# Kernel optimization log

Hardware: AMD Instinct MI355X
Metric: run time of the kernel (lower is better)

Reference implementation:

```python
import jax, jax.numpy as jnp
import numpy as np

N = 50000      # nodes (== nbr_nodes)
E = 800000     # edges
D_IN = 128
D_H = 128
D_OUT = 47
NOISE_RATE = 0.1
EPS = 1e-12


def _lin_init(key, out_f, in_f):
    # rough Glorot-style init for a PyG Linear weight [out_f, in_f]
    s = 1.0 / np.sqrt(in_f)
    return jax.random.uniform(key, (out_f, in_f), jnp.float32, -s, s)


def setup_inputs() -> dict:
    key = jax.random.key(0)
    ks = jax.random.split(key, 13)
    inp = {
        "x": jax.random.normal(ks[0], (N, D_IN), jnp.float32),
        "edge_index": jax.random.randint(ks[1], (2, E), 0, N, dtype=jnp.int32),
        "noise": jax.random.normal(ks[2], (N, D_IN), jnp.float32),
        # layer 0: in -> hidden
        "W_l0": _lin_init(ks[3], D_H, D_IN),
        "b_l0": jnp.zeros((D_H,), jnp.float32),
        "W_r0": _lin_init(ks[4], D_H, D_IN),
        # layer 1: hidden -> hidden
        "W_l1": _lin_init(ks[5], D_H, D_H),
        "b_l1": jnp.zeros((D_H,), jnp.float32),
        "W_r1": _lin_init(ks[6], D_H, D_H),
        # layer 2: hidden -> out
        "W_l2": _lin_init(ks[7], D_OUT, D_H),
        "b_l2": jnp.zeros((D_OUT,), jnp.float32),
        "W_r2": _lin_init(ks[8], D_OUT, D_H),
    }
    return inp


def _sage_conv(x, src, dst, W_l, b_l, W_r):
    # PyG SAGEConv with mean aggregation:
    #   out_i = W_l @ mean_{j in N(i)} x_j + b_l + W_r @ x_i
    msg = x[src]                                              # [E, d] gather
    ssum = jax.ops.segment_sum(msg, dst, num_segments=N)      # [N, d]
    cnt = jax.ops.segment_sum(jnp.ones((src.shape[0], 1), x.dtype), dst,
                              num_segments=N)                 # [N, 1]
    agg = ssum / jnp.maximum(cnt, 1.0)                        # mean; 0 for isolated nodes
    return agg @ W_l.T + b_l + x @ W_r.T


def _branch(x, src, dst, params):
    # stacked SAGEConv; relu after all but last layer; dropout is identity (eval mode)
    h = None
    n_layers = len(params)
    for i, (W_l, b_l, W_r) in enumerate(params):
        x = _sage_conv(x, src, dst, W_l, b_l, W_r)
        if i != n_layers - 1:
            x = jax.nn.relu(x)
            h = x
    return h, jax.nn.log_softmax(x, axis=1), x


def _add_noise(x, noise):
    # n_id=None path: x + sign(x) * F.normalize(noise, dim=1) * noise_rate
    norm = jnp.sqrt(jnp.sum(noise * noise, axis=1, keepdims=True))
    unit = noise / jnp.maximum(norm, EPS)
    return x + jnp.sign(x) * unit * NOISE_RATE


def reference(x, edge_index, noise,
              W_l0, b_l0, W_r0, W_l1, b_l1, W_r1, W_l2, b_l2, W_r2):
    src, dst = edge_index[0], edge_index[1]
    params = [(W_l0, b_l0, W_r0), (W_l1, b_l1, W_r1), (W_l2, b_l2, W_r2)]
    h_p, y_p, z_p = _branch(x, src, dst, params)
    h_n, y_n, z_n = _branch(_add_noise(x, noise), src, dst, params)
    return (h_p, y_p, z_p, h_n, y_n, z_n)
```

## Files before the change

### kernel.cpp

```cpp
#include <hip/hip_runtime.h>
#include <math.h>


typedef unsigned int uint;
typedef unsigned short ushort;
typedef unsigned char uchar;
typedef short bf16x8 __attribute__((ext_vector_type(8)));
typedef float f32x4 __attribute__((ext_vector_type(4)));

__device__ __forceinline__ ushort f2b(float f) {
  union { float f; uint u; } v; v.f = f;
  uint u = v.u;
  return (ushort)((u + 0x7FFFu + ((u >> 16) & 1u)) >> 16);
}
__device__ __forceinline__ float b2f_lo(uint u) {
  union { uint u; float f; } v; v.u = u << 16; return v.f;
}
__device__ __forceinline__ float b2f_hi(uint u) {
  union { uint u; float f; } v; v.u = u & 0xFFFF0000u; return v.f;
}

#if __has_builtin(__builtin_amdgcn_cvt_f32_fp8)
__device__ __forceinline__ float dec8_0(uint u) { return __builtin_amdgcn_cvt_f32_fp8(u, 0); }
__device__ __forceinline__ float dec8_1(uint u) { return __builtin_amdgcn_cvt_f32_fp8(u, 1); }
__device__ __forceinline__ float dec8_2(uint u) { return __builtin_amdgcn_cvt_f32_fp8(u, 2); }
__device__ __forceinline__ float dec8_3(uint u) { return __builtin_amdgcn_cvt_f32_fp8(u, 3); }
#else
__device__ __forceinline__ float dec8_b(uint b) {
  uint s = (b >> 7) & 1u, ex = (b >> 3) & 0xFu, m = b & 7u;
  union { uint u; float f; } v;
  if (ex == 0) {
    v.f = (float)m * 0.001953125f;
    v.u |= s << 31;
    return v.f;
  }
  v.u = (s << 31) | ((ex + 120u) << 23) | (m << 20);
  return v.f;
}
__device__ __forceinline__ float dec8_0(uint u) { return dec8_b(u & 0xFFu); }
__device__ __forceinline__ float dec8_1(uint u) { return dec8_b((u >> 8) & 0xFFu); }
__device__ __forceinline__ float dec8_2(uint u) { return dec8_b((u >> 16) & 0xFFu); }
__device__ __forceinline__ float dec8_3(uint u) { return dec8_b((u >> 24) & 0xFFu); }
#endif

#if __has_builtin(__builtin_amdgcn_cvt_pk_fp8_f32)
__device__ __forceinline__ uchar enc8(float f) {
  return (uchar)(__builtin_amdgcn_cvt_pk_fp8_f32(f, f, 0u, false) & 0xFFu);
}
#else
__device__ __forceinline__ uchar enc8(float f) {
  union { float f; uint u; } v; v.f = f;
  uint s = v.u >> 31;
  uint a = v.u & 0x7FFFFFFFu;
  if (a >= 0x43E00000u) return (uchar)((s << 7) | 0x7Eu);
  if (a < 0x3C800000u) {
    float q = fabsf(f) * 512.0f;
    uint m = (uint)(q + 0.5f);
    return (uchar)((s << 7) | m);
  }
  uint r = a + 0x00080000u;
  if (r >= 0x43E00000u) return (uchar)((s << 7) | 0x7Eu);
  uint ex = (r >> 23) - 120u;
  uint m = (r >> 20) & 7u;
  return (uchar)((s << 7) | (ex << 3) | m);
}
#endif

__global__ __launch_bounds__(256) void count_kernel(
    const int* __restrict__ dst, int* __restrict__ cnt,
    int* __restrict__ rank, int E) {
  int e = blockIdx.x * blockDim.x + threadIdx.x;
  if (e >= E) return;
  rank[e] = atomicAdd(&cnt[dst[e]], 1);
}

__global__ __launch_bounds__(256) void scan_blocks(
    const int* __restrict__ cnt, int* __restrict__ loc,
    int* __restrict__ bsum, int n) {
  __shared__ int ls[4];
  int t = threadIdx.x;
  int base = blockIdx.x * 1024 + t * 4;
  int v[4];
  int s = 0;
#pragma unroll
  for (int i = 0; i < 4; ++i) {
    v[i] = (base + i < n) ? cnt[base + i] : 0;
    s += v[i];
  }
  int lane = t & 63, wid = t >> 6;
  int ps = s;
#pragma unroll
  for (int d = 1; d < 64; d <<= 1) {
    int o = __shfl_up(ps, d, 64);
    if (lane >= d) ps += o;
  }
  if (lane == 63) ls[wid] = ps;
  __syncthreads();
  if (t == 0) {
    int r = 0;
#pragma unroll
    for (int w = 0; w < 4; ++w) { int x = ls[w]; ls[w] = r; r += x; }
  }
  __syncthreads();
  int run = ps - s + ls[wid];
#pragma unroll
  for (int i = 0; i < 4; ++i) {
    if (base + i < n) loc[base + i] = run;
    run += v[i];
  }
  if (t == 255) bsum[blockIdx.x] = ps + ls[wid];
}

__global__ __launch_bounds__(256) void scan_bsums(int* __restrict__ bsum,
                                                  int nb) {
  __shared__ int ls[4];
  int t = threadIdx.x;
  int v = (t < nb) ? bsum[t] : 0;
  int lane = t & 63, wid = t >> 6;
  int ps = v;
#pragma unroll
  for (int d = 1; d < 64; d <<= 1) {
    int o = __shfl_up(ps, d, 64);
    if (lane >= d) ps += o;
  }
  if (lane == 63) ls[wid] = ps;
  __syncthreads();
  if (t == 0) {
    int r = 0;
#pragma unroll
    for (int w = 0; w < 4; ++w) { int x = ls[w]; ls[w] = r; r += x; }
  }
  __syncthreads();
  if (t < nb) bsum[t] = ps - v + ls[wid];
}

__global__ __launch_bounds__(256) void scan_apply(
    const int* __restrict__ loc, const int* __restrict__ bsum,
    int* __restrict__ off, int n, int E) {
  int i = blockIdx.x * 256 + threadIdx.x;
  if (i < n) off[i] = loc[i] + bsum[i >> 10];
  if (i == 0) off[n] = E;
}

__global__ __launch_bounds__(256) void fill_kernel(
    const int* __restrict__ src, const int* __restrict__ dst,
    const int* __restrict__ rank, const int* __restrict__ off,
    int* __restrict__ csr, int E) {
  int e = blockIdx.x * blockDim.x + threadIdx.x;
  if (e >= E) return;
  csr[off[dst[e]] + rank[e]] = src[e];
}

__global__ __launch_bounds__(256) void noisy_convert(
    const float* __restrict__ x, const float* __restrict__ noise,
    ushort* __restrict__ XB, int N) {
  int node = (blockIdx.x * blockDim.x + threadIdx.x) >> 6;
  int lane = threadIdx.x & 63;
  if (node >= N) return;
  size_t base = (size_t)node * 128 + 2 * lane;
  float2 nz = *(const float2*)(noise + base);
  float ss = nz.x * nz.x + nz.y * nz.y;
#pragma unroll
  for (int m = 1; m < 64; m <<= 1) ss += __shfl_xor(ss, m, 64);
  float scale = 0.1f / fmaxf(sqrtf(ss), 1e-12f);
  float2 xv = *(const float2*)(x + base);
  float s0 = (xv.x > 0.f) ? 1.f : ((xv.x < 0.f) ? -1.f : 0.f);
  float s1 = (xv.y > 0.f) ? 1.f : ((xv.y < 0.f) ? -1.f : 0.f);
  float n0 = xv.x + s0 * nz.x * scale;
  float n1 = xv.y + s1 * nz.y * scale;
  uint pc = ((uint)f2b(xv.y) << 16) | f2b(xv.x);
  uint pn = ((uint)f2b(n1) << 16) | f2b(n0);
  *(uint*)(XB + (size_t)(2 * node) * 128 + 2 * lane) = pc;
  *(uint*)(XB + (size_t)(2 * node + 1) * 128 + 2 * lane) = pn;
}

__global__ __launch_bounds__(256) void conv_weights(
    const float* __restrict__ Wl0, const float* __restrict__ Wr0,
    const float* __restrict__ Wl1, const float* __restrict__ Wr1,
    const float* __restrict__ Wl2, const float* __restrict__ Wr2,
    ushort* __restrict__ WB0, ushort* __restrict__ WB1,
    ushort* __restrict__ WB2) {
  int i = blockIdx.x * 256 + threadIdx.x;
  if (i < 16384) {
    WB0[i] = f2b(Wl0[i]);
    WB0[16384 + i] = f2b(Wr0[i]);
    WB1[i] = f2b(Wl1[i]);
    WB1[16384 + i] = f2b(Wr1[i]);
  }
  if (i < 6016) {
    WB2[i] = f2b(Wl2[i]);
    WB2[6016 + i] = f2b(Wr2[i]);
  }
}

__global__ __launch_bounds__(512) void gemm_fused(
    const ushort* __restrict__ A, const ushort* __restrict__ W,
    uchar* __restrict__ P8, float* __restrict__ Rf, int M) {
  __shared__ ushort As[128 * 72];
  __shared__ ushort Ws[256 * 72];
  int tid = threadIdx.x;
  int lane = tid & 63, wid = tid >> 6;
  int wm = wid & 1, wn = wid >> 1;
  int lrow = lane & 15, quad = lane >> 4;
  int row0 = blockIdx.x * 128;

  f32x4 acc[4][4];
#pragma unroll
  for (int mt = 0; mt < 4; ++mt)
#pragma unroll
    for (int nt = 0; nt < 4; ++nt) acc[mt][nt] = (f32x4)(0.f);

  for (int k0 = 0; k0 < 128; k0 += 64) {
    for (int c = tid; c < 128 * 8; c += 512) {
      int r = c >> 3, kc = c & 7;
      int gr = row0 + r;
      uint4 v = make_uint4(0, 0, 0, 0);
      if (gr < M) v = *(const uint4*)(A + (size_t)gr * 128 + k0 + kc * 8);
      *(uint4*)(As + r * 72 + kc * 8) = v;
    }
    for (int c = tid; c < 256 * 8; c += 512) {
      int r = c >> 3, kc = c & 7;
      uint4 v = *(const uint4*)(W + (size_t)r * 128 + k0 + kc * 8);
      *(uint4*)(Ws + r * 72 + kc * 8) = v;
    }
    __syncthreads();
#pragma unroll
    for (int ks = 0; ks < 64; ks += 32) {
      bf16x8 af[4], bw[4];
#pragma unroll
      for (int mt = 0; mt < 4; ++mt)
        af[mt] = *(const bf16x8*)(As + (wm * 64 + mt * 16 + lrow) * 72 + ks + quad * 8);
#pragma unroll
      for (int nt = 0; nt < 4; ++nt)
        bw[nt] = *(const bf16x8*)(Ws + (wn * 64 + nt * 16 + lrow) * 72 + ks + quad * 8);
#pragma unroll
      for (int mt = 0; mt < 4; ++mt)
#pragma unroll
        for (int nt = 0; nt < 4; ++nt)
          acc[mt][nt] = __builtin_amdgcn_mfma_f32_16x16x32_bf16(
              af[mt], bw[nt], acc[mt][nt], 0, 0, 0);
    }
    __syncthreads();
  }
  if (wn < 2) {
#pragma unroll
    for (int mt = 0; mt < 4; ++mt) {
#pragma unroll
      for (int nt = 0; nt < 4; ++nt) {
        int col = wn * 64 + nt * 16 + lrow;
#pragma unroll
        for (int rg = 0; rg < 4; rg += 2) {
          int row = row0 + wm * 64 + mt * 16 + quad * 4 + rg;
          if (row >= M) continue;
          int nd = row >> 1;
          float cv = acc[mt][nt][rg];
          float nv = acc[mt][nt][rg + 1];
          uchar c8 = enc8(cv);
          float cr = dec8_0((uint)c8);
          P8[(size_t)nd * 256 + col] = c8;
          P8[(size_t)nd * 256 + 128 + col] = enc8(nv - cr);
        }
      }
    }
  } else {
#pragma unroll
    for (int mt = 0; mt < 4; ++mt) {
#pragma unroll
      for (int nt = 0; nt < 4; ++nt) {
        int colR = (wn - 2) * 64 + nt * 16 + lrow;
#pragma unroll
        for (int rg = 0; rg < 4; ++rg) {
          int row = row0 + wm * 64 + mt * 16 + quad * 4 + rg;
          if (row >= M) continue;
          int nd = row >> 1, hf = row & 1;
          Rf[(size_t)nd * 256 + hf * 128 + colR] = acc[mt][nt][rg];
        }
      }
    }
  }
}

__global__ __launch_bounds__(256) void gemm_l2(
    const ushort* __restrict__ A, const ushort* __restrict__ W,
    ushort* __restrict__ Pzc, uchar* __restrict__ Pzd,
    float* __restrict__ Rz, int M) {
  constexpr int NT = 3;
  __shared__ ushort As[128 * 72];
  __shared__ ushort Ws[96 * 72];
  int tid = threadIdx.x;
  int lane = tid & 63, wid = tid >> 6;
  int wm = wid & 1, wn = wid >> 1;
  int lrow = lane & 15, quad = lane >> 4;
  int row0 = blockIdx.x * 128;

  f32x4 acc[4][NT];
#pragma unroll
  for (int mt = 0; mt < 4; ++mt)
#pragma unroll
    for (int nt = 0; nt < NT; ++nt) acc[mt][nt] = (f32x4)(0.f);

  for (int k0 = 0; k0 < 128; k0 += 64) {
    for (int c = tid; c < 128 * 8; c += 256) {
      int r = c >> 3, kc = c & 7;
      int gr = row0 + r;
      uint4 v = make_uint4(0, 0, 0, 0);
      if (gr < M) v = *(const uint4*)(A + (size_t)gr * 128 + k0 + kc * 8);
      *(uint4*)(As + r * 72 + kc * 8) = v;
    }
    for (int c = tid; c < 96 * 8; c += 256) {
      int r = c >> 3, kc = c & 7;
      uint4 v = make_uint4(0, 0, 0, 0);
      if (r < 94) v = *(const uint4*)(W + (size_t)r * 128 + k0 + kc * 8);
      *(uint4*)(Ws + r * 72 + kc * 8) = v;
    }
    __syncthreads();
#pragma unroll
    for (int ks = 0; ks < 64; ks += 32) {
      bf16x8 af[4], bw[NT];
#pragma unroll
      for (int mt = 0; mt < 4; ++mt)
        af[mt] = *(const bf16x8*)(As + (wm * 64 + mt * 16 + lrow) * 72 + ks + quad * 8);
#pragma unroll
      for (int nt = 0; nt < NT; ++nt)
        bw[nt] = *(const bf16x8*)(Ws + (wn * NT * 16 + nt * 16 + lrow) * 72 + ks + quad * 8);
#pragma unroll
      for (int mt = 0; mt < 4; ++mt)
#pragma unroll
        for (int nt = 0; nt < NT; ++nt)
          acc[mt][nt] = __builtin_amdgcn_mfma_f32_16x16x32_bf16(
              af[mt], bw[nt], acc[mt][nt], 0, 0, 0);
    }
    __syncthreads();
  }
#pragma unroll
  for (int mt = 0; mt < 4; ++mt) {
#pragma unroll
    for (int nt = 0; nt < NT; ++nt) {
      int col = wn * NT * 16 + nt * 16 + lrow;
#pragma unroll
      for (int rg = 0; rg < 4; rg += 2) {
        int row = row0 + wm * 64 + mt * 16 + quad * 4 + rg;
        if (row >= M) continue;
        int nd = row >> 1;
        float cv = acc[mt][nt][rg];
        float nv = acc[mt][nt][rg + 1];
        if (col < 47) {
          ushort cb = f2b(cv);
          Pzc[(size_t)nd * 64 + col] = cb;
          Pzd[(size_t)nd * 64 + col] = enc8(nv - b2f_lo((uint)cb));
        } else if (col < 94) {
          Rz[(size_t)nd * 128 + (col - 47)] = cv;
          Rz[(size_t)nd * 128 + 64 + (col - 47)] = nv;
        }
      }
    }
  }
}

template <bool WF32>
__global__ __launch_bounds__(256) void agg_dual128(
    const uchar* __restrict__ P8, const float* __restrict__ R2,
    const float* __restrict__ bias, const int* __restrict__ off,
    const int* __restrict__ csr, float* __restrict__ f0,
    float* __restrict__ f1, ushort* __restrict__ bout, int N) {
  int node = (blockIdx.x * blockDim.x + threadIdx.x) >> 6;
  int lane = threadIdx.x & 63;
  if (node >= N) return;
  int lq = lane & 31;
  int b = off[node], e = off[node + 1];
  float s0 = 0.f, s1 = 0.f, s2 = 0.f, s3 = 0.f;
  float t0 = 0.f, t1 = 0.f, t2 = 0.f, t3 = 0.f;
  int j = b;
  for (; j + 8 <= e; j += 8) {
    int a0 = csr[j],     a1 = csr[j + 1], a2 = csr[j + 2], a3 = csr[j + 3];
    int a4 = csr[j + 4], a5 = csr[j + 5], a6 = csr[j + 6], a7 = csr[j + 7];
    uint u0 = *(const uint*)(P8 + (size_t)a0 * 256 + 4 * lane);
    uint u1 = *(const uint*)(P8 + (size_t)a1 * 256 + 4 * lane);
    uint u2 = *(const uint*)(P8 + (size_t)a2 * 256 + 4 * lane);
    uint u3 = *(const uint*)(P8 + (size_t)a3 * 256 + 4 * lane);
    uint u4 = *(const uint*)(P8 + (size_t)a4 * 256 + 4 * lane);
    uint u5 = *(const uint*)(P8 + (size_t)a5 * 256 + 4 * lane);
    uint u6 = *(const uint*)(P8 + (size_t)a6 * 256 + 4 * lane);
    uint u7 = *(const uint*)(P8 + (size_t)a7 * 256 + 4 * lane);
    s0 += dec8_0(u0) + dec8_0(u1) + dec8_0(u2) + dec8_0(u3);
    s1 += dec8_1(u0) + dec8_1(u1) + dec8_1(u2) + dec8_1(u3);
    s2 += dec8_2(u0) + dec8_2(u1) + dec8_2(u2) + dec8_2(u3);
    s3 += dec8_3(u0) + dec8_3(u1) + dec8_3(u2) + dec8_3(u3);
    t0 += dec8_0(u4) + dec8_0(u5) + dec8_0(u6) + dec8_0(u7);
    t1 += dec8_1(u4) + dec8_1(u5) + dec8_1(u6) + dec8_1(u7);
    t2 += dec8_2(u4) + dec8_2(u5) + dec8_2(u6) + dec8_2(u7);
    t3 += dec8_3(u4) + dec8_3(u5) + dec8_3(u6) + dec8_3(u7);
  }
  if (j + 4 <= e) {
    int a0 = csr[j], a1 = csr[j + 1], a2 = csr[j + 2], a3 = csr[j + 3];
    uint u0 = *(const uint*)(P8 + (size_t)a0 * 256 + 4 * lane);
    uint u1 = *(const uint*)(P8 + (size_t)a1 * 256 + 4 * lane);
    uint u2 = *(const uint*)(P8 + (size_t)a2 * 256 + 4 * lane);
    uint u3 = *(const uint*)(P8 + (size_t)a3 * 256 + 4 * lane);
    s0 += dec8_0(u0) + dec8_0(u1) + dec8_0(u2) + dec8_0(u3);
    s1 += dec8_1(u0) + dec8_1(u1) + dec8_1(u2) + dec8_1(u3);
    s2 += dec8_2(u0) + dec8_2(u1) + dec8_2(u2) + dec8_2(u3);
    s3 += dec8_3(u0) + dec8_3(u1) + dec8_3(u2) + dec8_3(u3);
    j += 4;
  }
  for (; j < e; ++j) {
    uint u0 = *(const uint*)(P8 + (size_t)csr[j] * 256 + 4 * lane);
    s0 += dec8_0(u0);
    s1 += dec8_1(u0);
    s2 += dec8_2(u0);
    s3 += dec8_3(u0);
  }
  s0 += t0; s1 += t1; s2 += t2; s3 += t3;
  float o0 = __shfl_xor(s0, 32, 64);
  float o1 = __shfl_xor(s1, 32, 64);
  float o2 = __shfl_xor(s2, 32, 64);
  float o3 = __shfl_xor(s3, 32, 64);
  bool hi = lane >= 32;
  float m0 = hi ? (s0 + o0) : s0;
  float m1 = hi ? (s1 + o1) : s1;
  float m2 = hi ? (s2 + o2) : s2;
  float m3 = hi ? (s3 + o3) : s3;
  float invd = 1.f / (float)max(e - b, 1);
  float4 rv = *(const float4*)(R2 + (size_t)node * 256 + 4 * lane);
  float4 bb = *(const float4*)(bias + 4 * lq);
  float q0 = fmaxf(m0 * invd + bb.x + rv.x, 0.f);
  float q1 = fmaxf(m1 * invd + bb.y + rv.y, 0.f);
  float q2 = fmaxf(m2 * invd + bb.z + rv.z, 0.f);
  float q3 = fmaxf(m3 * invd + bb.w + rv.w, 0.f);
  size_t arow = (size_t)(2 * node + (hi ? 1 : 0)) * 128 + 4 * lq;
  ushort4 pk;
  pk.x = f2b(q0); pk.y = f2b(q1); pk.z = f2b(q2); pk.w = f2b(q3);
  *(ushort4*)(bout + arow) = pk;
  if (WF32) {
    float* dst = (hi ? f1 : f0) + (size_t)node * 128 + 4 * lq;
    *(float4*)dst = make_float4(q0, q1, q2, q3);
  }
}

__global__ __launch_bounds__(256) void agg47_dual(
    const ushort* __restrict__ Pzc, const uchar* __restrict__ Pzd,
    const float* __restrict__ Rz, const float* __restrict__ bias,
    const int* __restrict__ off, const int* __restrict__ csr,
    float* __restrict__ z0, float* __restrict__ z1, float* __restrict__ y0,
    float* __restrict__ y1, int N) {
  int node = (blockIdx.x * blockDim.x + threadIdx.x) >> 6;
  int lane = threadIdx.x & 63;
  if (node >= N) return;
  int lq = lane & 31;
  int b = off[node], e = off[node + 1];
  float a = 0.f, aa = 0.f;
  float g0 = 0.f, g1 = 0.f;
  float h0 = 0.f, h1 = 0.f;
  int j = b;
  for (; j + 8 <= e; j += 8) {
    int a0 = csr[j],     a1 = csr[j + 1], a2 = csr[j + 2], a3 = csr[j + 3];
    int a4 = csr[j + 4], a5 = csr[j + 5], a6 = csr[j + 6], a7 = csr[j + 7];
    uint c0 = Pzc[(size_t)a0 * 64 + lane];
    uint c1 = Pzc[(size_t)a1 * 64 + lane];
    uint c2 = Pzc[(size_t)a2 * 64 + lane];
    uint c3 = Pzc[(size_t)a3 * 64 + lane];
    uint c4 = Pzc[(size_t)a4 * 64 + lane];
    uint c5 = Pzc[(size_t)a5 * 64 + lane];
    uint c6 = Pzc[(size_t)a6 * 64 + lane];
    uint c7 = Pzc[(size_t)a7 * 64 + lane];
    uint d0 = *(const ushort*)(Pzd + (size_t)a0 * 64 + 2 * lq);
    uint d1 = *(const ushort*)(Pzd + (size_t)a1 * 64 + 2 * lq);
    uint d2 = *(const ushort*)(Pzd + (size_t)a2 * 64 + 2 * lq);
    uint d3 = *(const ushort*)(Pzd + (size_t)a3 * 64 + 2 * lq);
    uint d4 = *(const ushort*)(Pzd + (size_t)a4 * 64 + 2 * lq);
    uint d5 = *(const ushort*)(Pzd + (size_t)a5 * 64 + 2 * lq);
    uint d6 = *(const ushort*)(Pzd + (size_t)a6 * 64 + 2 * lq);
    uint d7 = *(const ushort*)(Pzd + (size_t)a7 * 64 + 2 * lq);
    a  += b2f_lo(c0) + b2f_lo(c1) + b2f_lo(c2) + b2f_lo(c3);
    aa += b2f_lo(c4) + b2f_lo(c5) + b2f_lo(c6) + b2f_lo(c7);
    g0 += dec8_0(d0) + dec8_0(d1) + dec8_0(d2) + dec8_0(d3);
    g1 += dec8_1(d0) + dec8_1(d1) + dec8_1(d2) + dec8_1(d3);
    h0 += dec8_0(d4) + dec8_0(d5) + dec8_0(d6) + dec8_0(d7);
    h1 += dec8_1(d4) + dec8_1(d5) + dec8_1(d6) + dec8_1(d7);
  }
  if (j + 4 <= e) {
    int a0 = csr[j], a1 = csr[j + 1], a2 = csr[j + 2], a3 = csr[j + 3];
    uint c0 = Pzc[(size_t)a0 * 64 + lane];
    uint c1 = Pzc[(size_t)a1 * 64 + lane];
    uint c2 = Pzc[(size_t)a2 * 64 + lane];
    uint c3 = Pzc[(size_t)a3 * 64 + lane];
    uint d0 = *(const ushort*)(Pzd + (size_t)a0 * 64 + 2 * lq);
    uint d1 = *(const ushort*)(Pzd + (size_t)a1 * 64 + 2 * lq);
    uint d2 = *(const ushort*)(Pzd + (size_t)a2 * 64 + 2 * lq);
    uint d3 = *(const ushort*)(Pzd + (size_t)a3 * 64 + 2 * lq);
    a  += b2f_lo(c0) + b2f_lo(c1) + b2f_lo(c2) + b2f_lo(c3);
    g0 += dec8_0(d0) + dec8_0(d1) + dec8_0(d2) + dec8_0(d3);
    g1 += dec8_1(d0) + dec8_1(d1) + dec8_1(d2) + dec8_1(d3);
    j += 4;
  }
  for (; j < e; ++j) {
    uint c0 = Pzc[(size_t)csr[j] * 64 + lane];
    uint d0 = *(const ushort*)(Pzd + (size_t)csr[j] * 64 + 2 * lq);
    a += b2f_lo(c0);
    g0 += dec8_0(d0);
    g1 += dec8_1(d0);
  }
  a += aa; g0 += h0; g1 += h1;
  float dd0 = __shfl(g0, lane >> 1, 64);
  float dd1 = __shfl(g1, lane >> 1, 64);
  float dl = (lane & 1) ? dd1 : dd0;
  bool v = lane < 47;
  float invd = 1.f / (float)max(e - b, 1);
  float rc = Rz[(size_t)node * 128 + lane];
  float rn = Rz[(size_t)node * 128 + 64 + lane];
  float bl = v ? bias[lane] : 0.f;
  float za = v ? (a * invd + bl + rc) : -INFINITY;
  float zn = v ? ((a + dl) * invd + bl + rn) : -INFINITY;
  float ma = za, mb = zn;
#pragma unroll
  for (int d = 1; d < 64; d <<= 1) {
    ma = fmaxf(ma, __shfl_xor(ma, d, 64));
    mb = fmaxf(mb, __shfl_xor(mb, d, 64));
  }
  float sa = v ? __expf(za - ma) : 0.f;
  float sb = v ? __expf(zn - mb) : 0.f;
#pragma unroll
  for (int d = 1; d < 64; d <<= 1) {
    sa += __shfl_xor(sa, d, 64);
    sb += __shfl_xor(sb, d, 64);
  }
  float lsa = logf(sa) + ma;
  float lsb = logf(sb) + mb;
  if (v) {
    z0[(size_t)node * 47 + lane] = za;
    y0[(size_t)node * 47 + lane] = za - lsa;
    z1[(size_t)node * 47 + lane] = zn;
    y1[(size_t)node * 47 + lane] = zn - lsb;
  }
}

extern "C" void kernel_launch(void* const* d_in, const int* in_sizes, int n_in,
                              void* d_out, int out_size, void* d_ws,
                              size_t ws_size, hipStream_t stream) {
  const float* x = (const float*)d_in[0];
  const int* ei = (const int*)d_in[1];
  const float* noise = (const float*)d_in[2];
  const float* Wl0 = (const float*)d_in[3];
  const float* bl0 = (const float*)d_in[4];
  const float* Wr0 = (const float*)d_in[5];
  const float* Wl1 = (const float*)d_in[6];
  const float* bl1 = (const float*)d_in[7];
  const float* Wr1 = (const float*)d_in[8];
  const float* Wl2 = (const float*)d_in[9];
  const float* bl2 = (const float*)d_in[10];
  const float* Wr2 = (const float*)d_in[11];

  const int N = in_sizes[0] / 128;
  const int E = in_sizes[1] / 2;
  const int M = 2 * N;

  float* out = (float*)d_out;
  float* h_p = out;
  float* y_p = h_p + (size_t)N * 128;
  float* z_p = y_p + (size_t)N * 47;
  float* h_n = z_p + (size_t)N * 47;
  float* y_n = h_n + (size_t)N * 128;
  float* z_n = y_n + (size_t)N * 47;

  char* w = (char*)d_ws;
  auto alloc = [&](size_t bytes) {
    void* p = (void*)w;
    w += (bytes + 511) & ~(size_t)511;
    return p;
  };
  ushort* XB = (ushort*)alloc((size_t)M * 128 * 2);
  uchar* P8 = (uchar*)alloc((size_t)N * 256);
  float* Rf = (float*)alloc((size_t)M * 128 * 4);
  ushort* WB0 = (ushort*)alloc(256 * 128 * 2);
  ushort* WB1 = (ushort*)alloc(256 * 128 * 2);
  ushort* WB2 = (ushort*)alloc(94 * 128 * 2);
  int* cnt = (int*)alloc((size_t)N * 4);
  int* off = (int*)alloc((size_t)(N + 1) * 4);
  int* rank = (int*)alloc((size_t)E * 4);
  int* loc = (int*)alloc((size_t)N * 4);
  int* bsum = (int*)alloc((size_t)256 * 4);
  int* csr = (int*)alloc((size_t)E * 4);
  ushort* Pzc = (ushort*)P8;
  uchar* Pzd = P8 + (size_t)N * 128;

  conv_weights<<<(16384 + 255) / 256, 256, 0, stream>>>(
      Wl0, Wr0, Wl1, Wr1, Wl2, Wr2, WB0, WB1, WB2);

  hipMemsetAsync(cnt, 0, (size_t)N * 4, stream);
  int eb = (E + 255) / 256;
  count_kernel<<<eb, 256, 0, stream>>>(ei + E, cnt, rank, E);
  int sb = (N + 1023) / 1024;
  scan_blocks<<<sb, 256, 0, stream>>>(cnt, loc, bsum, N);
  scan_bsums<<<1, 256, 0, stream>>>(bsum, sb);
  scan_apply<<<(N + 255) / 256, 256, 0, stream>>>(loc, bsum, off, N, E);
  fill_kernel<<<eb, 256, 0, stream>>>(ei, ei + E, rank, off, csr, E);

  int nwb = (N + 3) / 4;
  int rb = (M + 127) / 128;

  noisy_convert<<<nwb, 256, 0, stream>>>(x, noise, XB, N);

  gemm_fused<<<rb, 512, 0, stream>>>(XB, WB0, P8, Rf, M);
  agg_dual128<false><<<nwb, 256, 0, stream>>>(P8, Rf, bl0, off, csr, nullptr,
                                              nullptr, XB, N);
  gemm_fused<<<rb, 512, 0, stream>>>(XB, WB1, P8, Rf, M);
  agg_dual128<true><<<nwb, 256, 0, stream>>>(P8, Rf, bl1, off, csr, h_p, h_n,
                                             XB, N);
  gemm_l2<<<rb, 256, 0, stream>>>(XB, WB2, Pzc, Pzd, Rf, M);
  agg47_dual<<<nwb, 256, 0, stream>>>(Pzc, Pzd, Rf, bl2, off, csr, z_p, z_n,
                                      y_p, y_n, N);
}
```

Baseline: 415.9 us.

## Fuse prep kernels, merge scan stages, store root term in bf16

Weight conversion, count zeroing and noisy input conversion are merged into one prep kernel, which replaces a memset and a separate launch. The block-sum scan is folded into scan_apply, so each block redundantly rescans the block sums instead of running a separate one-block kernel. The root-term buffer for the two 128-wide layers is now stored in bf16, halving that traffic, while layer 2 keeps a separate fp32 buffer. This trades fewer launches and less memory traffic for some extra rounding in the hidden layers.

```diff
diff --git a/kernel.cpp b/kernel.cpp
--- a/kernel.cpp
+++ b/kernel.cpp
@@ -66,96 +66,32 @@
 }
 #endif
 
-__global__ __launch_bounds__(256) void count_kernel(
-    const int* __restrict__ dst, int* __restrict__ cnt,
-    int* __restrict__ rank, int E) {
-  int e = blockIdx.x * blockDim.x + threadIdx.x;
-  if (e >= E) return;
-  rank[e] = atomicAdd(&cnt[dst[e]], 1);
-}
-
-__global__ __launch_bounds__(256) void scan_blocks(
-    const int* __restrict__ cnt, int* __restrict__ loc,
-    int* __restrict__ bsum, int n) {
-  __shared__ int ls[4];
-  int t = threadIdx.x;
-  int base = blockIdx.x * 1024 + t * 4;
-  int v[4];
-  int s = 0;
-#pragma unroll
-  for (int i = 0; i < 4; ++i) {
-    v[i] = (base + i < n) ? cnt[base + i] : 0;
-    s += v[i];
-  }
-  int lane = t & 63, wid = t >> 6;
-  int ps = s;
-#pragma unroll
-  for (int d = 1; d < 64; d <<= 1) {
-    int o = __shfl_up(ps, d, 64);
-    if (lane >= d) ps += o;
-  }
-  if (lane == 63) ls[wid] = ps;
-  __syncthreads();
-  if (t == 0) {
-    int r = 0;
-#pragma unroll
-    for (int w = 0; w < 4; ++w) { int x = ls[w]; ls[w] = r; r += x; }
-  }
-  __syncthreads();
-  int run = ps - s + ls[wid];
-#pragma unroll
-  for (int i = 0; i < 4; ++i) {
-    if (base + i < n) loc[base + i] = run;
-    run += v[i];
-  }
-  if (t == 255) bsum[blockIdx.x] = ps + ls[wid];
-}
-
-__global__ __launch_bounds__(256) void scan_bsums(int* __restrict__ bsum,
-                                                  int nb) {
-  __shared__ int ls[4];
-  int t = threadIdx.x;
-  int v = (t < nb) ? bsum[t] : 0;
-  int lane = t & 63, wid = t >> 6;
-  int ps = v;
-#pragma unroll
-  for (int d = 1; d < 64; d <<= 1) {
-    int o = __shfl_up(ps, d, 64);
-    if (lane >= d) ps += o;
-  }
-  if (lane == 63) ls[wid] = ps;
-  __syncthreads();
-  if (t == 0) {
-    int r = 0;
-#pragma unroll
-    for (int w = 0; w < 4; ++w) { int x = ls[w]; ls[w] = r; r += x; }
-  }
-  __syncthreads();
-  if (t < nb) bsum[t] = ps - v + ls[wid];
-}
-
-__global__ __launch_bounds__(256) void scan_apply(
-    const int* __restrict__ loc, const int* __restrict__ bsum,
-    int* __restrict__ off, int n, int E) {
-  int i = blockIdx.x * 256 + threadIdx.x;
-  if (i < n) off[i] = loc[i] + bsum[i >> 10];
-  if (i == 0) off[n] = E;
-}
-
-__global__ __launch_bounds__(256) void fill_kernel(
-    const int* __restrict__ src, const int* __restrict__ dst,
-    const int* __restrict__ rank, const int* __restrict__ off,
-    int* __restrict__ csr, int E) {
-  int e = blockIdx.x * blockDim.x + threadIdx.x;
-  if (e >= E) return;
-  csr[off[dst[e]] + rank[e]] = src[e];
-}
-
-__global__ __launch_bounds__(256) void noisy_convert(
+__global__ __launch_bounds__(256) void prep_kernel(
     const float* __restrict__ x, const float* __restrict__ noise,
-    ushort* __restrict__ XB, int N) {
-  int node = (blockIdx.x * blockDim.x + threadIdx.x) >> 6;
-  int lane = threadIdx.x & 63;
+    ushort* __restrict__ XB,
+    const float* __restrict__ Wl0, const float* __restrict__ Wr0,
+    const float* __restrict__ Wl1, const float* __restrict__ Wr1,
+    const float* __restrict__ Wl2, const float* __restrict__ Wr2,
+    ushort* __restrict__ WB0, ushort* __restrict__ WB1,
+    ushort* __restrict__ WB2, int* __restrict__ cnt, int N) {
+  int blk = blockIdx.x, t = threadIdx.x;
+  if (blk < 64) {
+    int i = blk * 256 + t;
+    WB0[i] = f2b(Wl0[i]);
+    WB0[16384 + i] = f2b(Wr0[i]);
+    WB1[i] = f2b(Wl1[i]);
+    WB1[16384 + i] = f2b(Wr1[i]);
+    if (i < 6016) {
+      WB2[i] = f2b(Wl2[i]);
+      WB2[6016 + i] = f2b(Wr2[i]);
+    }
+  }
+  {
+    int i = blk * 256 + t;
+    if (i < N) cnt[i] = 0;
+  }
+  int node = (blk * 256 + t) >> 6;
+  int lane = t & 63;
   if (node >= N) return;
   size_t base = (size_t)node * 128 + 2 * lane;
   float2 nz = *(const float2*)(noise + base);
@@ -174,28 +110,92 @@
   *(uint*)(XB + (size_t)(2 * node + 1) * 128 + 2 * lane) = pn;
 }
 
-__global__ __launch_bounds__(256) void conv_weights(
-    const float* __restrict__ Wl0, const float* __restrict__ Wr0,
-    const float* __restrict__ Wl1, const float* __restrict__ Wr1,
-    const float* __restrict__ Wl2, const float* __restrict__ Wr2,
-    ushort* __restrict__ WB0, ushort* __restrict__ WB1,
-    ushort* __restrict__ WB2) {
-  int i = blockIdx.x * 256 + threadIdx.x;
-  if (i < 16384) {
-    WB0[i] = f2b(Wl0[i]);
-    WB0[16384 + i] = f2b(Wr0[i]);
-    WB1[i] = f2b(Wl1[i]);
-    WB1[16384 + i] = f2b(Wr1[i]);
-  }
-  if (i < 6016) {
-    WB2[i] = f2b(Wl2[i]);
-    WB2[6016 + i] = f2b(Wr2[i]);
-  }
+__global__ __launch_bounds__(256) void count_kernel(
+    const int* __restrict__ dst, int* __restrict__ cnt,
+    int* __restrict__ rank, int E) {
+  int e = blockIdx.x * blockDim.x + threadIdx.x;
+  if (e >= E) return;
+  rank[e] = atomicAdd(&cnt[dst[e]], 1);
+}
+
+__global__ __launch_bounds__(256) void scan_blocks(
+    const int* __restrict__ cnt, int* __restrict__ loc,
+    int* __restrict__ bsum, int n) {
+  __shared__ int ls[4];
+  int t = threadIdx.x;
+  int base = blockIdx.x * 1024 + t * 4;
+  int v[4];
+  int s = 0;
+#pragma unroll
+  for (int i = 0; i < 4; ++i) {
+    v[i] = (base + i < n) ? cnt[base + i] : 0;
+    s += v[i];
+  }
+  int lane = t & 63, wid = t >> 6;
+  int ps = s;
+#pragma unroll
+  for (int d = 1; d < 64; d <<= 1) {
+    int o = __shfl_up(ps, d, 64);
+    if (lane >= d) ps += o;
+  }
+  if (lane == 63) ls[wid] = ps;
+  __syncthreads();
+  if (t == 0) {
+    int r = 0;
+#pragma unroll
+    for (int w = 0; w < 4; ++w) { int x = ls[w]; ls[w] = r; r += x; }
+  }
+  __syncthreads();
+  int run = ps - s + ls[wid];
+#pragma unroll
+  for (int i = 0; i < 4; ++i) {
+    if (base + i < n) loc[base + i] = run;
+    run += v[i];
+  }
+  if (t == 255) bsum[blockIdx.x] = ps + ls[wid];
+}
+
+__global__ __launch_bounds__(256) void scan_apply(
+    const int* __restrict__ loc, const int* __restrict__ bsum,
+    int* __restrict__ off, int n, int E, int nb) {
+  __shared__ int ls[4];
+  __shared__ int ex[256];
+  int t = threadIdx.x;
+  int v = (t < nb) ? bsum[t] : 0;
+  int lane = t & 63, wid = t >> 6;
+  int ps = v;
+#pragma unroll
+  for (int d = 1; d < 64; d <<= 1) {
+    int o = __shfl_up(ps, d, 64);
+    if (lane >= d) ps += o;
+  }
+  if (lane == 63) ls[wid] = ps;
+  __syncthreads();
+  if (t == 0) {
+    int r = 0;
+#pragma unroll
+    for (int w = 0; w < 4; ++w) { int x = ls[w]; ls[w] = r; r += x; }
+  }
+  __syncthreads();
+  ex[t] = ps - v + ls[wid];
+  __syncthreads();
+  int i = blockIdx.x * 256 + t;
+  if (i < n) off[i] = loc[i] + ex[i >> 10];
+  if (i == 0) off[n] = E;
+}
+
+__global__ __launch_bounds__(256) void fill_kernel(
+    const int* __restrict__ src, const int* __restrict__ dst,
+    const int* __restrict__ rank, const int* __restrict__ off,
+    int* __restrict__ csr, int E) {
+  int e = blockIdx.x * blockDim.x + threadIdx.x;
+  if (e >= E) return;
+  csr[off[dst[e]] + rank[e]] = src[e];
 }
 
 __global__ __launch_bounds__(512) void gemm_fused(
     const ushort* __restrict__ A, const ushort* __restrict__ W,
-    uchar* __restrict__ P8, float* __restrict__ Rf, int M) {
+    uchar* __restrict__ P8, ushort* __restrict__ Rb, int M) {
   __shared__ ushort As[128 * 72];
   __shared__ ushort Ws[256 * 72];
   int tid = threadIdx.x;
@@ -273,7 +273,7 @@
           int row = row0 + wm * 64 + mt * 16 + quad * 4 + rg;
           if (row >= M) continue;
           int nd = row >> 1, hf = row & 1;
-          Rf[(size_t)nd * 256 + hf * 128 + colR] = acc[mt][nt][rg];
+          Rb[(size_t)nd * 256 + hf * 128 + colR] = f2b(acc[mt][nt][rg]);
         }
       }
     }
@@ -359,7 +359,7 @@
 
 template <bool WF32>
 __global__ __launch_bounds__(256) void agg_dual128(
-    const uchar* __restrict__ P8, const float* __restrict__ R2,
+    const uchar* __restrict__ P8, const ushort* __restrict__ Rb,
     const float* __restrict__ bias, const int* __restrict__ off,
     const int* __restrict__ csr, float* __restrict__ f0,
     float* __restrict__ f1, ushort* __restrict__ bout, int N) {
@@ -421,12 +421,14 @@
   float m2 = hi ? (s2 + o2) : s2;
   float m3 = hi ? (s3 + o3) : s3;
   float invd = 1.f / (float)max(e - b, 1);
-  float4 rv = *(const float4*)(R2 + (size_t)node * 256 + 4 * lane);
+  uint2 rp = *(const uint2*)(Rb + (size_t)node * 256 + 4 * lane);
+  float rvx = b2f_lo(rp.x), rvy = b2f_hi(rp.x);
+  float rvz = b2f_lo(rp.y), rvw = b2f_hi(rp.y);
   float4 bb = *(const float4*)(bias + 4 * lq);
-  float q0 = fmaxf(m0 * invd + bb.x + rv.x, 0.f);
-  float q1 = fmaxf(m1 * invd + bb.y + rv.y, 0.f);
-  float q2 = fmaxf(m2 * invd + bb.z + rv.z, 0.f);
-  float q3 = fmaxf(m3 * invd + bb.w + rv.w, 0.f);
+  float q0 = fmaxf(m0 * invd + bb.x + rvx, 0.f);
+  float q1 = fmaxf(m1 * invd + bb.y + rvy, 0.f);
+  float q2 = fmaxf(m2 * invd + bb.z + rvz, 0.f);
+  float q3 = fmaxf(m3 * invd + bb.w + rvw, 0.f);
   size_t arow = (size_t)(2 * node + (hi ? 1 : 0)) * 128 + 4 * lq;
   ushort4 pk;
   pk.x = f2b(q0); pk.y = f2b(q1); pk.z = f2b(q2); pk.w = f2b(q3);
@@ -494,8 +496,9 @@
     j += 4;
   }
   for (; j < e; ++j) {
-    uint c0 = Pzc[(size_t)csr[j] * 64 + lane];
-    uint d0 = *(const ushort*)(Pzd + (size_t)csr[j] * 64 + 2 * lq);
+    int a0 = csr[j];
+    uint c0 = Pzc[(size_t)a0 * 64 + lane];
+    uint d0 = *(const ushort*)(Pzd + (size_t)a0 * 64 + 2 * lq);
     a += b2f_lo(c0);
     g0 += dec8_0(d0);
     g1 += dec8_1(d0);
@@ -570,7 +573,8 @@
   };
   ushort* XB = (ushort*)alloc((size_t)M * 128 * 2);
   uchar* P8 = (uchar*)alloc((size_t)N * 256);
-  float* Rf = (float*)alloc((size_t)M * 128 * 4);
+  ushort* Rb = (ushort*)alloc((size_t)M * 128 * 2);
+  float* Rz = (float*)alloc((size_t)N * 128 * 4);
   ushort* WB0 = (ushort*)alloc(256 * 128 * 2);
   ushort* WB1 = (ushort*)alloc(256 * 128 * 2);
   ushort* WB2 = (ushort*)alloc(94 * 128 * 2);
@@ -583,30 +587,26 @@
   ushort* Pzc = (ushort*)P8;
   uchar* Pzd = P8 + (size_t)N * 128;
 
-  conv_weights<<<(16384 + 255) / 256, 256, 0, stream>>>(
-      Wl0, Wr0, Wl1, Wr1, Wl2, Wr2, WB0, WB1, WB2);
-
-  hipMemsetAsync(cnt, 0, (size_t)N * 4, stream);
-  int eb = (E + 255) / 256;
-  count_kernel<<<eb, 256, 0, stream>>>(ei + E, cnt, rank, E);
-  int sb = (N + 1023) / 1024;
-  scan_blocks<<<sb, 256, 0, stream>>>(cnt, loc, bsum, N);
-  scan_bsums<<<1, 256, 0, stream>>>(bsum, sb);
-  scan_apply<<<(N + 255) / 256, 256, 0, stream>>>(loc, bsum, off, N, E);
-  fill_kernel<<<eb, 256, 0, stream>>>(ei, ei + E, rank, off, csr, E);
-
   int nwb = (N + 3) / 4;
   int rb = (M + 127) / 128;
-
-  noisy_convert<<<nwb, 256, 0, stream>>>(x, noise, XB, N);
-
-  gemm_fused<<<rb, 512, 0, stream>>>(XB, WB0, P8, Rf, M);
-  agg_dual128<false><<<nwb, 256, 0, stream>>>(P8, Rf, bl0, off, csr, nullptr,
+  int eb = (E + 255) / 256;
+  int sb = (N + 1023) / 1024;
+
+  prep_kernel<<<nwb, 256, 0, stream>>>(x, noise, XB, Wl0, Wr0, Wl1, Wr1, Wl2,
+                                       Wr2, WB0, WB1, WB2, cnt, N);
+
+  count_kernel<<<eb, 256, 0, stream>>>(ei + E, cnt, rank, E);
+  scan_blocks<<<sb, 256, 0, stream>>>(cnt, loc, bsum, N);
+  scan_apply<<<(N + 255) / 256, 256, 0, stream>>>(loc, bsum, off, N, E, sb);
+  fill_kernel<<<eb, 256, 0, stream>>>(ei, ei + E, rank, off, csr, E);
+
+  gemm_fused<<<rb, 512, 0, stream>>>(XB, WB0, P8, Rb, M);
+  agg_dual128<false><<<nwb, 256, 0, stream>>>(P8, Rb, bl0, off, csr, nullptr,
                                               nullptr, XB, N);
-  gemm_fused<<<rb, 512, 0, stream>>>(XB, WB1, P8, Rf, M);
-  agg_dual128<true><<<nwb, 256, 0, stream>>>(P8, Rf, bl1, off, csr, h_p, h_n,
+  gemm_fused<<<rb, 512, 0, stream>>>(XB, WB1, P8, Rb, M);
+  agg_dual128<true><<<nwb, 256, 0, stream>>>(P8, Rb, bl1, off, csr, h_p, h_n,
                                              XB, N);
-  gemm_l2<<<rb, 256, 0, stream>>>(XB, WB2, Pzc, Pzd, Rf, M);
-  agg47_dual<<<nwb, 256, 0, stream>>>(Pzc, Pzd, Rf, bl2, off, csr, z_p, z_n,
+  gemm_l2<<<rb, 256, 0, stream>>>(XB, WB2, Pzc, Pzd, Rz, M);
+  agg47_dual<<<nwb, 256, 0, stream>>>(Pzc, Pzd, Rz, bl2, off, csr, z_p, z_n,
                                       y_p, y_n, N);
 }
```

Measured after the change: 414.0 us. No clear change (-0.5%).
